# Optimization experiments

Measured on AMD Instinct MI355X. Metric: run time of the kernel, lower is better.

The kernel has to match this reference:

```python
import jax, jax.numpy as jnp
import numpy as np

K = 3
STRIDE = 1
PAD = 1
GROUPS = 16
EPS = 1e-5


def _conv2d(x, w, b, stride, pad):
    out = jax.lax.conv_general_dilated(
        x, w, (stride, stride), [(pad, pad), (pad, pad)],
        dimension_numbers=("NCHW", "OIHW", "NCHW"))
    return out + b[None, :, None, None]


def setup_inputs() -> dict:
    key = jax.random.key(0)
    ks = jax.random.split(key, 6)
    B, Cin, H, W = 4, 256, 64, 64
    Cout = 256
    x = jax.random.normal(ks[0], (B, Cin, H, W), dtype=jnp.float32)
    # DCNv2 offset/mask-generating conv: 3*K*K = 27 output channels
    w_off = jax.random.normal(ks[1], (3 * K * K, Cin, K, K), dtype=jnp.float32) * 0.01
    b_off = jnp.zeros((3 * K * K,), dtype=jnp.float32)
    # main deformable conv weight/bias
    weight = jax.random.normal(ks[2], (Cout, Cin, K, K), dtype=jnp.float32) * 0.02
    bias = jnp.zeros((Cout,), dtype=jnp.float32)
    # GroupNorm affine params
    gamma = jnp.ones((Cout,), dtype=jnp.float32)
    beta = jnp.zeros((Cout,), dtype=jnp.float32)
    return {"x": x, "w_off": w_off, "b_off": b_off,
            "weight": weight, "bias": bias, "gamma": gamma, "beta": beta}


def reference(x, w_off, b_off, weight, bias, gamma, beta):
    B, Cin, H, W = x.shape
    Cout = weight.shape[0]
    KK = K * K

    # --- offset/mask branch (DCNv2): 18 offsets + 9 sigmoid masks ---
    om = _conv2d(x, w_off, b_off, STRIDE, PAD)          # [B, 27, Ho, Wo]
    Ho, Wo = om.shape[2], om.shape[3]
    off_y, off_x, m = jnp.split(om, 3, axis=1)          # each [B, 9, Ho, Wo]
    mask = jax.nn.sigmoid(m)

    # --- sampling coordinates: base grid + kernel tap + learned offset ---
    kgy = jnp.repeat(jnp.arange(K, dtype=x.dtype), K)   # [9] row of tap
    kgx = jnp.tile(jnp.arange(K, dtype=x.dtype), K)     # [9] col of tap
    base_y = jnp.arange(Ho, dtype=x.dtype) * STRIDE - PAD
    base_x = jnp.arange(Wo, dtype=x.dtype) * STRIDE - PAD
    py = base_y[None, None, :, None] + kgy[None, :, None, None] + off_y  # [B,9,Ho,Wo]
    px = base_x[None, None, None, :] + kgx[None, :, None, None] + off_x  # [B,9,Ho,Wo]

    # --- bilinear sampling with zero padding outside the image ---
    y0 = jnp.floor(py)
    x0 = jnp.floor(px)
    wy1 = py - y0
    wx1 = px - x0

    def gather(img, yy, xx):
        # img [Cin,H,W], yy/xx [9,Ho,Wo] int -> [Cin,9,Ho,Wo]
        return img[:, yy, xx]

    def corner(yi, xi, wy, wx):
        valid = (yi >= 0) & (yi < H) & (xi >= 0) & (xi < W)
        yc = jnp.clip(yi, 0, H - 1).astype(jnp.int32)
        xc = jnp.clip(xi, 0, W - 1).astype(jnp.int32)
        vals = jax.vmap(gather)(x, yc, xc)               # [B,Cin,9,Ho,Wo]
        w_ = (wy * wx * valid.astype(x.dtype))[:, None]   # [B,1,9,Ho,Wo]
        return vals * w_

    sampled = (corner(y0, x0, (1 - wy1), (1 - wx1))
               + corner(y0, x0 + 1, (1 - wy1), wx1)
               + corner(y0 + 1, x0, wy1, (1 - wx1))
               + corner(y0 + 1, x0 + 1, wy1, wx1))       # [B,Cin,9,Ho,Wo]
    sampled = sampled * mask[:, None]                     # modulation

    # --- conv accumulation over taps and input channels ---
    out = jnp.einsum("bckhw,ock->bohw", sampled,
                     weight.reshape(Cout, Cin, KK)) + bias[None, :, None, None]

    # --- GroupNorm(16, Cout) ---
    og = out.reshape(B, GROUPS, Cout // GROUPS, Ho, Wo)
    mu = og.mean(axis=(2, 3, 4), keepdims=True)
    var = og.var(axis=(2, 3, 4), keepdims=True)
    og = (og - mu) * jax.lax.rsqrt(var + EPS)
    out = og.reshape(B, Cout, Ho, Wo) * gamma[None, :, None, None] + beta[None, :, None, None]
    return out
```

## Files before the change

### kernel.cpp

```cpp
#include <hip/hip_runtime.h>
#include <math.h>

#define CIN   256
#define COUT  256
#define H     64
#define W     64
#define HW    4096
#define KK    9
#define KC    2304
#define NOFF  27
#define B_    4
#define EPS   1e-5f
#define OM3S  (B_ * NOFF * HW)

typedef __attribute__((ext_vector_type(4))) float f32x4;
typedef __attribute__((ext_vector_type(8))) short s16x8;

static __device__ __forceinline__ unsigned short f2bf(float f) {
  unsigned u = __builtin_bit_cast(unsigned, f);
  u += 0x7FFF + ((u >> 16) & 1);
  return (unsigned short)(u >> 16);
}
static __device__ __forceinline__ float bflo(unsigned u) {
  return __builtin_bit_cast(float, u << 16);
}
static __device__ __forceinline__ float bfhi(unsigned u) {
  return __builtin_bit_cast(float, u & 0xffff0000u);
}
static __device__ __forceinline__ unsigned packbf(float lo, float hi) {
  unsigned ul = __builtin_bit_cast(unsigned, lo);
  unsigned uh = __builtin_bit_cast(unsigned, hi);
  ul += 0x7FFF + ((ul >> 16) & 1);
  uh += 0x7FFF + ((uh >> 16) & 1);
  return (ul >> 16) | (uh & 0xffff0000u);
}

__global__ __launch_bounds__(256) void prep_kernel(
    const float* __restrict__ x, const float* __restrict__ w,
    const float* __restrict__ w_off, unsigned short* __restrict__ xT,
    unsigned short* __restrict__ wBf, unsigned short* __restrict__ wOBf,
    float* __restrict__ gstat) {
  int bi = blockIdx.x;
  int t = threadIdx.x;
  if (bi < 256) {
    __shared__ unsigned short tile[64][272];
    int b = bi >> 6, y = bi & 63;
    const float* src = x + (size_t)b * CIN * HW + y * W;
    for (int r = 0; r < 64; ++r) {
      int idx = r * 256 + t;
      int c = idx >> 6, ww = idx & 63;
      tile[ww][c] = f2bf(src[(size_t)c * HW + ww]);
    }
    __syncthreads();
    unsigned short* dst = xT + ((size_t)(b * 64 + y) * 64) * 256;
    for (int r = 0; r < 8; ++r) {
      int idx = r * 2048 + t * 8;
      int ww = idx >> 8, c = idx & 255;
      *(uint4*)(dst + idx) = *(const uint4*)&tile[ww][c];
    }
  } else if (bi < 544) {
    int pkt = (bi - 256) * 256 + t;
    int lane = pkt & 63;
    int tn = (pkt >> 6) & 15;
    int k2 = pkt >> 10;
    int co = tn * 16 + (lane & 15);
    int kb = k2 * 32 + (lane >> 4) * 8;
    unsigned short v[8];
#pragma unroll
    for (int j = 0; j < 8; ++j) {
      int kk = kb + j;
      int kt = kk >> 8, c = kk & 255;
      v[j] = f2bf(w[(co * 256 + c) * 9 + kt]);
    }
    *(uint4*)&wBf[(size_t)pkt * 8] = *(const uint4*)v;
  } else if (bi < 580) {
    int pkt = (bi - 544) * 256 + t;
    int lane = pkt & 63;
    int tn = (pkt >> 6) & 1;
    int k2 = pkt >> 7;
    int oc = tn * 16 + (lane & 15);
    int kb = k2 * 32 + (lane >> 4) * 8;
    unsigned short v[8];
#pragma unroll
    for (int j = 0; j < 8; ++j) {
      int kk = kb + j;
      int kt = kk >> 8, c = kk & 255;
      v[j] = (oc < NOFF) ? f2bf(w_off[(oc * 256 + c) * 9 + kt]) : (unsigned short)0;
    }
    *(uint4*)&wOBf[(size_t)pkt * 8] = *(const uint4*)v;
  } else {
    if (t < 128) gstat[t] = 0.f;
  }
}

__global__ __launch_bounds__(256) void offconv_mfma_kernel(
    const unsigned short* __restrict__ xT, const unsigned short* __restrict__ wOBf,
    float* __restrict__ om3) {
  int bi = blockIdx.x;
  int ts = bi >> 8;
  int row = bi & 255;
  int b = row >> 6, i = row & 63;
  int t = threadIdx.x, lane = t & 63, wv = t >> 6;
  int lr = lane & 15, lq = lane >> 4;
  int p = wv * 16 + lr;
  const unsigned short* xb = xT + (size_t)b * (HW * 256);
  f32x4 acc[2] = {};

  for (int kc = 0; kc < 3; ++kc) {
    int kt = ts * 3 + kc;
    int ky = kt / 3, kx = kt % 3;
    int yy = i - 1 + ky, xx = p - 1 + kx;
    bool ok = ((unsigned)yy < 64u) && ((unsigned)xx < 64u);
    const unsigned short* ap = xb + ((ok ? yy * 64 + xx : 0) << 8) + lq * 8;
#pragma unroll
    for (int c8 = 0; c8 < 8; ++c8) {
      uint4 av = uint4{0, 0, 0, 0};
      if (ok) av = *(const uint4*)(ap + c8 * 32);
      int k2 = kt * 8 + c8;
      s16x8 a = __builtin_bit_cast(s16x8, av);
      s16x8 b0 = *(const s16x8*)(wOBf + ((((k2 * 2 + 0) << 6) | lane) << 3));
      s16x8 b1 = *(const s16x8*)(wOBf + ((((k2 * 2 + 1) << 6) | lane) << 3));
      acc[0] = __builtin_amdgcn_mfma_f32_16x16x32_bf16(a, b0, acc[0], 0, 0, 0);
      acc[1] = __builtin_amdgcn_mfma_f32_16x16x32_bf16(a, b1, acc[1], 0, 0, 0);
    }
  }
#pragma unroll
  for (int tn = 0; tn < 2; ++tn) {
    int oc = tn * 16 + lr;
    if (oc < NOFF) {
      float* ob = om3 + (size_t)ts * OM3S + ((b * NOFF + oc) << 12) + i * 64 + wv * 16;
#pragma unroll
      for (int r = 0; r < 4; ++r) ob[lq * 4 + r] = acc[tn][r];
    }
  }
}

__global__ __launch_bounds__(512, 2) void gemm_fused_kernel(
    const unsigned short* __restrict__ xT, const float* __restrict__ om3,
    const float* __restrict__ b_off, const unsigned short* __restrict__ wBf,
    const float* __restrict__ bias, unsigned short* __restrict__ cvt,
    float* __restrict__ gstat) {
  __shared__ float tapw[64][KK][4];
  __shared__ int   tapc[64][KK][4];
  __shared__ unsigned short At[2][64 * 64];
  int mt = blockIdx.x;
  int m0 = mt * 64;
  int b = m0 >> 12;
  int irow = (m0 & 4095) >> 6;
  int t = threadIdx.x;
  int lane = t & 63, wv = t >> 6;
  int lr = lane & 15, lq = lane >> 4;
  const unsigned short* xb = xT + (size_t)b * (HW * 256);

  for (int idx = t; idx < 64 * KK; idx += 512) {
    int p = idx / KK, k = idx % KK;
    int pix = (m0 & 4095) + p;
    size_t o = (size_t)(b * NOFF) * HW + pix;
    float offy = om3[o + k * HW] + om3[OM3S + o + k * HW] +
                 om3[2 * OM3S + o + k * HW] + b_off[k];
    float offx = om3[o + (9 + k) * HW] + om3[OM3S + o + (9 + k) * HW] +
                 om3[2 * OM3S + o + (9 + k) * HW] + b_off[9 + k];
    float mval = om3[o + (18 + k) * HW] + om3[OM3S + o + (18 + k) * HW] +
                 om3[2 * OM3S + o + (18 + k) * HW] + b_off[18 + k];
    float mask = 1.f / (1.f + __expf(-mval));
    float py = (float)(irow - 1 + k / 3) + offy;
    float px = (float)(p - 1 + k % 3) + offx;
    float y0f = floorf(py), x0f = floorf(px);
    float wy1 = py - y0f, wx1 = px - x0f;
    int y0 = (int)y0f, x0 = (int)x0f;
    bool y0ok = (unsigned)y0 < 64u, y1ok = (unsigned)(y0 + 1) < 64u;
    bool x0ok = (unsigned)x0 < 64u, x1ok = (unsigned)(x0 + 1) < 64u;
    tapw[p][k][0] = (1.f - wy1) * (1.f - wx1) * mask * (float)(y0ok && x0ok);
    tapw[p][k][1] = (1.f - wy1) * wx1 * mask * (float)(y0ok && x1ok);
    tapw[p][k][2] = wy1 * (1.f - wx1) * mask * (float)(y1ok && x0ok);
    tapw[p][k][3] = wy1 * wx1 * mask * (float)(y1ok && x1ok);
    int y0c = min(max(y0, 0), 63), y1c = min(max(y0 + 1, 0), 63);
    int x0c = min(max(x0, 0), 63), x1c = min(max(x0 + 1, 0), 63);
    tapc[p][k][0] = (y0c * 64 + x0c) * 256;
    tapc[p][k][1] = (x1c - x0c) * 256;
    tapc[p][k][2] = (y1c - y0c) * 64 * 256;
    tapc[p][k][3] = 0;
  }
  __syncthreads();

  bool isProd = (wv < 4);
  int p = (t & 255) >> 2, q = t & 3;
  int cw = isProd ? 0 : (wv - 4);
  const unsigned short* bb = wBf + ((size_t)(cw * 4) * 64 + lane) * 8;

  f32x4 acc[4][4] = {};
  s16x8 Bfa[2][4], Bfb[2][4];
  uint4 sG[8];

#define GLOAD(JJ)                                                            \
  {                                                                          \
    int kt_ = (JJ) >> 2, cg_ = (JJ) & 3;                                     \
    int4 tc_ = *(const int4*)&tapc[p][kt_][0];                               \
    const unsigned short* c_ = xb + tc_.x + cg_ * 64 + q * 16;               \
    sG[0] = *(const uint4*)(c_);                                             \
    sG[1] = *(const uint4*)(c_ + 8);                                         \
    sG[2] = *(const uint4*)(c_ + tc_.y);                                     \
    sG[3] = *(const uint4*)(c_ + tc_.y + 8);                                 \
    sG[4] = *(const uint4*)(c_ + tc_.z);                                     \
    sG[5] = *(const uint4*)(c_ + tc_.z + 8);                                 \
    sG[6] = *(const uint4*)(c_ + tc_.z + tc_.y);                             \
    sG[7] = *(const uint4*)(c_ + tc_.z + tc_.y + 8);                         \
  }

#define COMBINE(JJ, BUFI)                                                    \
  {                                                                          \
    int kt_ = (JJ) >> 2;                                                     \
    f32x4 tw_ = *(const f32x4*)&tapw[p][kt_][0];                             \
    _Pragma("unroll") for (int o = 0; o < 2; ++o) {                          \
      const unsigned* a00_ = (const unsigned*)&sG[0 + o];                    \
      const unsigned* a01_ = (const unsigned*)&sG[2 + o];                    \
      const unsigned* a10_ = (const unsigned*)&sG[4 + o];                    \
      const unsigned* a11_ = (const unsigned*)&sG[6 + o];                    \
      uint4 res_;                                                            \
      unsigned* rr_ = (unsigned*)&res_;                                      \
      _Pragma("unroll") for (int u = 0; u < 4; ++u) {                        \
        float lo_ = tw_[0] * bflo(a00_[u]) + tw_[1] * bflo(a01_[u]) +        \
                    tw_[2] * bflo(a10_[u]) + tw_[3] * bflo(a11_[u]);         \
        float hi_ = tw_[0] * bfhi(a00_[u]) + tw_[1] * bfhi(a01_[u]) +        \
                    tw_[2] * bfhi(a10_[u]) + tw_[3] * bfhi(a11_[u]);         \
        rr_[u] = packbf(lo_, hi_);                                           \
      }                                                                      \
      *(uint4*)((char*)At[BUFI] + p * 128 + (((q * 2 + o) ^ (p & 7)) * 16)) = res_; \
    }                                                                        \
  }

#define BISSUE(J, SLOT)                                                      \
  {                                                                          \
    int k2b_ = (J) * 2;                                                      \
    _Pragma("unroll") for (int kh = 0; kh < 2; ++kh)                         \
      _Pragma("unroll") for (int tn = 0; tn < 4; ++tn)                       \
        SLOT[kh][tn] = *(const s16x8*)(bb + (size_t)(k2b_ + kh) * 8192 + tn * 512); \
  }

#define CONSUME(BUFI, SLOT)                                                  \
  {                                                                          \
    const char* buf_ = (const char*)At[BUFI];                                \
    _Pragma("unroll") for (int kh = 0; kh < 2; ++kh) {                       \
      s16x8 af[4];                                                           \
      _Pragma("unroll") for (int tm = 0; tm < 4; ++tm) {                     \
        int r_ = tm * 16 + lr;                                               \
        af[tm] = *(const s16x8*)(buf_ + r_ * 128 + (((kh * 4 + lq) ^ (r_ & 7)) * 16)); \
      }                                                                      \
      __builtin_amdgcn_s_setprio(1);                                         \
      _Pragma("unroll") for (int tm = 0; tm < 4; ++tm)                       \
        _Pragma("unroll") for (int tn = 0; tn < 4; ++tn)                     \
          acc[tm][tn] = __builtin_amdgcn_mfma_f32_16x16x32_bf16(             \
              af[tm], SLOT[kh][tn], acc[tm][tn], 0, 0, 0);                   \
      __builtin_amdgcn_s_setprio(0);                                         \
    }                                                                        \
  }

#define SOFTBAR()                                                            \
  {                                                                          \
    asm volatile("s_waitcnt lgkmcnt(0)" ::: "memory");                       \
    __builtin_amdgcn_sched_barrier(0);                                       \
    __builtin_amdgcn_s_barrier();                                            \
  }

  if (isProd) {
    GLOAD(0);
    COMBINE(0, 0);
    GLOAD(1);
  } else {
    BISSUE(0, Bfa);
    BISSUE(1, Bfb);
  }
  SOFTBAR();

#pragma unroll 1
  for (int k = 0; k < 36; k += 2) {
    if (isProd) {
      COMBINE(k + 1, 1);
      if (k + 2 < 36) GLOAD(k + 2);
    } else {
      CONSUME(0, Bfa);
      if (k + 2 < 36) BISSUE(k + 2, Bfa);
    }
    SOFTBAR();
    if (isProd) {
      if (k + 2 < 36) COMBINE(k + 2, 0);
      if (k + 3 < 36) GLOAD(k + 3);
    } else {
      CONSUME(1, Bfb);
      if (k + 3 < 36) BISSUE(k + 3, Bfb);
    }
    SOFTBAR();
  }

#undef GLOAD
#undef COMBINE
#undef BISSUE
#undef CONSUME
#undef SOFTBAR

  if (!isProd) {
    int poff = m0 & 4095;
#pragma unroll
    for (int tn = 0; tn < 4; ++tn) {
      int co = cw * 64 + tn * 16 + lr;
      float bco = bias[co];
      unsigned short* cvb = cvt + (size_t)(b * COUT + co) * HW + poff;
      float sS = 0.f, qq = 0.f;
#pragma unroll
      for (int tm = 0; tm < 4; ++tm) {
        ushort4 st;
#pragma unroll
        for (int r = 0; r < 4; ++r) {
          float v = acc[tm][tn][r] + bco;
          sS += v;
          qq += v * v;
          ((unsigned short*)&st)[r] = f2bf(v);
        }
        *(ushort4*)(cvb + tm * 16 + lq * 4) = st;
      }
#pragma unroll
      for (int off = 32; off > 0; off >>= 1) {
        sS += __shfl_down(sS, off, 64);
        qq += __shfl_down(qq, off, 64);
      }
      if (lane == 0) {
        int g = co >> 4;
        atomicAdd(&gstat[(b * 16 + g) * 2 + 0], sS);
        atomicAdd(&gstat[(b * 16 + g) * 2 + 1], qq);
      }
    }
  }
}

__global__ __launch_bounds__(256) void gn_apply_kernel(
    const unsigned short* __restrict__ convout, const float* __restrict__ gstat,
    const float* __restrict__ gamma, const float* __restrict__ beta,
    float* __restrict__ out) {
  int vid = blockIdx.x * 256 + threadIdx.x;
  int e = vid * 8;
  int b = e >> 20;
  int c = (e >> 12) & 255;
  int g = c >> 4;
  float S = gstat[(b * 16 + g) * 2 + 0];
  float Q = gstat[(b * 16 + g) * 2 + 1];
  float mu = S * (1.f / 65536.f);
  float var = Q * (1.f / 65536.f) - mu * mu;
  float rs = rsqrtf(var + EPS);
  float a = rs * gamma[c];
  float bb = beta[c] - mu * a;
  uint4 v = *(const uint4*)(convout + e);
  const unsigned* u = (const unsigned*)&v;
  float4 o0, o1;
  o0.x = bflo(u[0]) * a + bb;  o0.y = bfhi(u[0]) * a + bb;
  o0.z = bflo(u[1]) * a + bb;  o0.w = bfhi(u[1]) * a + bb;
  o1.x = bflo(u[2]) * a + bb;  o1.y = bfhi(u[2]) * a + bb;
  o1.z = bflo(u[3]) * a + bb;  o1.w = bfhi(u[3]) * a + bb;
  *(float4*)(out + e) = o0;
  *(float4*)(out + e + 4) = o1;
}

extern "C" void kernel_launch(void* const* d_in, const int* in_sizes, int n_in,
                              void* d_out, int out_size, void* d_ws, size_t ws_size,
                              hipStream_t stream) {
  const float* x      = (const float*)d_in[0];
  const float* w_off  = (const float*)d_in[1];
  const float* b_off  = (const float*)d_in[2];
  const float* weight = (const float*)d_in[3];
  const float* bias   = (const float*)d_in[4];
  const float* gamma  = (const float*)d_in[5];
  const float* beta   = (const float*)d_in[6];
  float* out = (float*)d_out;

  float* om3 = (float*)d_ws;
  unsigned short* xT   = (unsigned short*)(om3 + (size_t)3 * OM3S);
  unsigned short* wBf  = xT + (size_t)B_ * HW * 256;
  unsigned short* wOBf = wBf + (size_t)COUT * KC;
  unsigned short* cvt  = wOBf + (size_t)32 * KC;
  float* gstat = (float*)(cvt + (size_t)B_ * HW * COUT);

  prep_kernel<<<dim3(581), dim3(256), 0, stream>>>(x, weight, w_off, xT, wBf, wOBf, gstat);
  offconv_mfma_kernel<<<dim3(768), dim3(256), 0, stream>>>(xT, wOBf, om3);
  gemm_fused_kernel<<<dim3(256), dim3(512), 0, stream>>>(xT, om3, b_off, wBf, bias, cvt, gstat);
  gn_apply_kernel<<<dim3(2048), dim3(256), 0, stream>>>(cvt, gstat, gamma, beta, out);
}
```

Baseline: 164.5 us.

## Process two K-steps per barrier with double-buffered A halves in producer/consumer GEMM

Restructures the warp-specialized producer/consumer loop so each barrier interval covers two K-slices. Producers gather and combine two slices into two halves of a double-buffered LDS tile, and consumers run MFMA over both. This halves the number of block barriers. It doubles the A-tile LDS and producer gather registers, and occupancy drops to one block per CU via launch bounds. Producers now issue GLOAD and immediately COMBINE within the same phase, so gather latency is no longer hidden across a barrier.

New measurement: 165.3 us. About the same (+0.4%).

```diff
diff --git a/kernel.cpp b/kernel.cpp
--- a/kernel.cpp
+++ b/kernel.cpp
@@ -135,14 +135,14 @@
   }
 }
 
-__global__ __launch_bounds__(512, 2) void gemm_fused_kernel(
+__global__ __launch_bounds__(512, 1) void gemm_fused_kernel(
     const unsigned short* __restrict__ xT, const float* __restrict__ om3,
     const float* __restrict__ b_off, const unsigned short* __restrict__ wBf,
     const float* __restrict__ bias, unsigned short* __restrict__ cvt,
     float* __restrict__ gstat) {
   __shared__ float tapw[64][KK][4];
   __shared__ int   tapc[64][KK][4];
-  __shared__ unsigned short At[2][64 * 64];
+  __shared__ unsigned short At[2][2][64 * 64];
   int mt = blockIdx.x;
   int m0 = mt * 64;
   int b = m0 >> 12;
@@ -190,32 +190,32 @@
 
   f32x4 acc[4][4] = {};
   s16x8 Bfa[2][4], Bfb[2][4];
-  uint4 sG[8];
-
-#define GLOAD(JJ)                                                            \
+  uint4 sGa[8], sGb[8];
+
+#define GLOAD(JJ, SLOT)                                                      \
   {                                                                          \
     int kt_ = (JJ) >> 2, cg_ = (JJ) & 3;                                     \
     int4 tc_ = *(const int4*)&tapc[p][kt_][0];                               \
     const unsigned short* c_ = xb + tc_.x + cg_ * 64 + q * 16;               \
-    sG[0] = *(const uint4*)(c_);                                             \
-    sG[1] = *(const uint4*)(c_ + 8);                                         \
-    sG[2] = *(const uint4*)(c_ + tc_.y);                                     \
-    sG[3] = *(const uint4*)(c_ + tc_.y + 8);                                 \
-    sG[4] = *(const uint4*)(c_ + tc_.z);                                     \
-    sG[5] = *(const uint4*)(c_ + tc_.z + 8);                                 \
-    sG[6] = *(const uint4*)(c_ + tc_.z + tc_.y);                             \
-    sG[7] = *(const uint4*)(c_ + tc_.z + tc_.y + 8);                         \
-  }
-
-#define COMBINE(JJ, BUFI)                                                    \
+    SLOT[0] = *(const uint4*)(c_);                                           \
+    SLOT[1] = *(const uint4*)(c_ + 8);                                       \
+    SLOT[2] = *(const uint4*)(c_ + tc_.y);                                   \
+    SLOT[3] = *(const uint4*)(c_ + tc_.y + 8);                               \
+    SLOT[4] = *(const uint4*)(c_ + tc_.z);                                   \
+    SLOT[5] = *(const uint4*)(c_ + tc_.z + 8);                               \
+    SLOT[6] = *(const uint4*)(c_ + tc_.z + tc_.y);                           \
+    SLOT[7] = *(const uint4*)(c_ + tc_.z + tc_.y + 8);                       \
+  }
+
+#define COMBINE(JJ, SLOT, BUFI, HALF)                                        \
   {                                                                          \
     int kt_ = (JJ) >> 2;                                                     \
     f32x4 tw_ = *(const f32x4*)&tapw[p][kt_][0];                             \
     _Pragma("unroll") for (int o = 0; o < 2; ++o) {                          \
-      const unsigned* a00_ = (const unsigned*)&sG[0 + o];                    \
-      const unsigned* a01_ = (const unsigned*)&sG[2 + o];                    \
-      const unsigned* a10_ = (const unsigned*)&sG[4 + o];                    \
-      const unsigned* a11_ = (const unsigned*)&sG[6 + o];                    \
+      const unsigned* a00_ = (const unsigned*)&SLOT[0 + o];                  \
+      const unsigned* a01_ = (const unsigned*)&SLOT[2 + o];                  \
+      const unsigned* a10_ = (const unsigned*)&SLOT[4 + o];                  \
+      const unsigned* a11_ = (const unsigned*)&SLOT[6 + o];                  \
       uint4 res_;                                                            \
       unsigned* rr_ = (unsigned*)&res_;                                      \
       _Pragma("unroll") for (int u = 0; u < 4; ++u) {                        \
@@ -225,7 +225,7 @@
                     tw_[2] * bfhi(a10_[u]) + tw_[3] * bfhi(a11_[u]);         \
         rr_[u] = packbf(lo_, hi_);                                           \
       }                                                                      \
-      *(uint4*)((char*)At[BUFI] + p * 128 + (((q * 2 + o) ^ (p & 7)) * 16)) = res_; \
+      *(uint4*)((char*)At[BUFI][HALF] + p * 128 + (((q * 2 + o) ^ (p & 7)) * 16)) = res_; \
     }                                                                        \
   }
 
@@ -237,9 +237,9 @@
         SLOT[kh][tn] = *(const s16x8*)(bb + (size_t)(k2b_ + kh) * 8192 + tn * 512); \
   }
 
-#define CONSUME(BUFI, SLOT)                                                  \
-  {                                                                          \
-    const char* buf_ = (const char*)At[BUFI];                                \
+#define CONSUME(BUFI, HALF, SLOT)                                            \
+  {                                                                          \
+    const char* buf_ = (const char*)At[BUFI][HALF];                          \
     _Pragma("unroll") for (int kh = 0; kh < 2; ++kh) {                       \
       s16x8 af[4];                                                           \
       _Pragma("unroll") for (int tm = 0; tm < 4; ++tm) {                     \
@@ -263,9 +263,10 @@
   }
 
   if (isProd) {
-    GLOAD(0);
-    COMBINE(0, 0);
-    GLOAD(1);
+    GLOAD(0, sGa);
+    GLOAD(1, sGb);
+    COMBINE(0, sGa, 0, 0);
+    COMBINE(1, sGb, 0, 1);
   } else {
     BISSUE(0, Bfa);
     BISSUE(1, Bfb);
@@ -273,21 +274,21 @@
   SOFTBAR();
 
 #pragma unroll 1
-  for (int k = 0; k < 36; k += 2) {
+  for (int j = 0; j < 18; ++j) {
     if (isProd) {
-      COMBINE(k + 1, 1);
-      if (k + 2 < 36) GLOAD(k + 2);
+      if (j < 17) {
+        GLOAD(2 * j + 2, sGa);
+        GLOAD(2 * j + 3, sGb);
+        COMBINE(2 * j + 2, sGa, (j + 1) & 1, 0);
+        COMBINE(2 * j + 3, sGb, (j + 1) & 1, 1);
+      }
     } else {
-      CONSUME(0, Bfa);
-      if (k + 2 < 36) BISSUE(k + 2, Bfa);
-    }
-    SOFTBAR();
-    if (isProd) {
-      if (k + 2 < 36) COMBINE(k + 2, 0);
-      if (k + 3 < 36) GLOAD(k + 3);
-    } else {
-      CONSUME(1, Bfb);
-      if (k + 3 < 36) BISSUE(k + 3, Bfb);
+      CONSUME(j & 1, 0, Bfa);
+      CONSUME(j & 1, 1, Bfb);
+      if (j < 17) {
+        BISSUE(2 * j + 2, Bfa);
+        BISSUE(2 * j + 3, Bfb);
+      }
     }
     SOFTBAR();
   }
```
